# Optimization experiments

Hardware: AMD Instinct MI355X
Metric: run time of the kernel (lower is better)

Reference implementation:

```python
import jax, jax.numpy as jnp
import numpy as np

N_STEPS = 96
BATCH = 16384
N_MAT = 8
N_STRIKES = 8
PERIOD = 12          # N_steps // n_maturities
T_HORIZON = 1.0
RFR = 0.03
S0 = 1.0
LAYER = 128
DT = T_HORIZON / N_STEPS
SQRT_DT = float(np.sqrt(DT))
DF = float(np.exp(-RFR * DT))  # per-step discount factor


def _mlp(Win, bin_, Wh, bh, Wout, bout, x, out_fn):
    # x: [features, batch]; linear layers act on axis 0 (matches torch cat along dim 0)
    h = jax.nn.leaky_relu(Win @ x + bin_[:, None])
    for k in range(Wh.shape[0]):
        h = jax.nn.leaky_relu(Wh[k] @ h + bh[k][:, None])
    return out_fn(Wout @ h + bout[:, None])


def _forward(normals, strikes, lev_Win, lev_bin, lev_Wh, lev_bh, lev_Wout, lev_bout,
             hed_Win, hed_bin, hed_Wh, hed_bh, hed_Wout, hed_bout):
    B = normals.shape[1]
    dt = jnp.float32(DT)
    sqrt_dt = jnp.float32(SQRT_DT)
    r = jnp.float32(RFR)
    df = jnp.float32(DF)
    sg = jax.lax.stop_gradient

    def body(carry, xs):
        S_prev, hedging, prices, variance = carry
        i, nn_i = xs                      # i: int32 step (1..N_STEPS), nn_i: [B] normals
        i_f = i.astype(jnp.float32)
        idx = (i - 1) // PERIOD           # which per-period MLP
        t = ((i_f - 1.0) * dt) * jnp.ones((1, B), jnp.float32)
        X = jnp.concatenate([t, S_prev], axis=0)          # [2, B]
        lev = _mlp(lev_Win[idx], lev_bin[idx], lev_Wh[idx], lev_bh[idx],
                   lev_Wout[idx], lev_bout[idx], X, jax.nn.softplus)  # [1, B]
        drift = S_prev * r / (1.0 + jnp.abs(sg(S_prev) * r) * sqrt_dt)
        diffusion = S_prev * lev / (1.0 + jnp.abs(sg(S_prev * lev)) * sqrt_dt)
        dW = sqrt_dt * nn_i                               # [B]
        S_curr = S_prev + drift * dt + diffusion * dW     # [1, B]
        Xh = jnp.concatenate([t, sg(S_prev)], axis=0)
        hedge = _mlp(hed_Win[idx], hed_bin[idx], hed_Wh[idx], hed_bh[idx],
                     hed_Wout[idx], hed_bout[idx], Xh,
                     lambda y: y).reshape(N_STRIKES, N_MAT, B)
        hedging = hedging + (df ** (i_f - 1.0)) * sg(S_prev * diffusion) * hedge * dW
        # maturity handling (maturities at steps PERIOD, 2*PERIOD, ..., N_STEPS)
        table_idx = jnp.clip(i // PERIOD - 1, 0, N_MAT - 1)
        is_mat = (i % PERIOD == 0).astype(jnp.float32)
        simulated = (df ** i_f) * jnp.maximum(S_curr - strikes[:, None], 0.0) \
                    - hedging[:, table_idx]               # [K, B]
        mean = simulated.mean(axis=1)                     # [K]
        var = jnp.sum((simulated - mean[:, None]) ** 2, axis=1) / (B - 1)  # unbiased, as torch .var()
        prices = prices.at[:, table_idx].add(is_mat * mean)
        variance = variance.at[:, table_idx].add(is_mat * var)
        return (S_curr, hedging, prices, variance), None

    body = jax.checkpoint(body)
    carry0 = (jnp.full((1, B), jnp.float32(S0)),
              jnp.zeros((N_STRIKES, N_MAT, B), jnp.float32),
              jnp.zeros((N_STRIKES, N_MAT), jnp.float32),
              jnp.zeros((N_STRIKES, N_MAT), jnp.float32))
    xs = (jnp.arange(1, N_STEPS + 1, dtype=jnp.int32), normals)
    (_, _, prices, variance), _ = jax.lax.scan(body, carry0, xs)
    return prices, variance


def setup_inputs() -> dict:
    key = jax.random.key(0)
    ks = jax.random.split(key, 16)
    M, L, NH = N_MAT, LAYER, 3  # num_layers=4 -> 3 hidden-to-hidden layers

    def w(k, shape, fan_in):
        return (jax.random.normal(k, shape, jnp.float32) / np.sqrt(fan_in)).astype(jnp.float32)

    inp = {
        "normals": jax.random.normal(ks[0], (N_STEPS, BATCH), jnp.float32),
        "strikes": jnp.linspace(0.8, 1.15, N_STRIKES, dtype=jnp.float32),
        "lev_Win": w(ks[1], (M, L, 2), 2),
        "lev_bin": w(ks[2], (M, L), L),
        "lev_Wh": w(ks[3], (M, NH, L, L), L),
        "lev_bh": w(ks[4], (M, NH, L), L),
        "lev_Wout": w(ks[5], (M, 1, L), L),
        "lev_bout": w(ks[6], (M, 1), L),
        "hed_Win": w(ks[7], (M, L, 2), 2),
        "hed_bin": w(ks[8], (M, L), L),
        "hed_Wh": w(ks[9], (M, NH, L, L), L),
        "hed_bh": w(ks[10], (M, NH, L), L),
        "hed_Wout": w(ks[11], (M, N_STRIKES * N_MAT, L), L),
        "hed_bout": w(ks[12], (M, N_STRIKES * N_MAT), L),
    }
    return inp


def reference(normals, strikes, lev_Win, lev_bin, lev_Wh, lev_bh, lev_Wout, lev_bout,
              hed_Win, hed_bin, hed_Wh, hed_bh, hed_Wout, hed_bout):
    return _forward(normals, strikes, lev_Win, lev_bin, lev_Wh, lev_bh, lev_Wout, lev_bout,
                    hed_Win, hed_bin, hed_Wh, hed_bh, hed_Wout, hed_bout)
```

## Files before the change

kernel.cpp:

```cpp
#include <hip/hip_runtime.h>
#include <math.h>

typedef __attribute__((ext_vector_type(8)))  short  short8;
typedef __attribute__((ext_vector_type(4)))  short  short4v;
typedef __attribute__((ext_vector_type(16))) float  f32x16;
typedef __attribute__((ext_vector_type(4)))  float  f32x4v;

#define DT_F    ((float)(1.0/96.0))
#define SQDT_F  (0.10206207261596575f)
#define DF_F    (0.99968754882437816f)
#define RFR_F   (0.03f)

#define SWZ(c,k) (((c)<<7) + ((k) ^ (((c)&15)<<3)))

static __device__ __forceinline__ short f2bf(float x) {
    return __builtin_bit_cast(short, (__bf16)x);
}
static __device__ __forceinline__ float bf2f(short h) {
    return (float)__builtin_bit_cast(__bf16, h);
}

__device__ __forceinline__ void layer1(const float* __restrict__ Win, const float* __restrict__ bin_,
        float t, const float* __restrict__ sScur, ushort* __restrict__ out, int wvm, int l)
{
    const int g = l >> 4, c15 = l & 15;
    const int r0 = (wvm << 5) + (g << 3);
    float a8[8], w1[8];
#pragma unroll
    for (int jj = 0; jj < 8; ++jj) {
        const int r = r0 + jj;
        a8[jj] = fmaf(Win[2*r], t, bin_[r]);
        w1[jj] = Win[2*r + 1];
    }
#pragma unroll
    for (int cc = 0; cc < 4; ++cc) {
        const int c = c15 + (cc << 4);
        const float S = sScur[c];
        short8 v;
#pragma unroll
        for (int jj = 0; jj < 8; ++jj) {
            float h = fmaf(w1[jj], S, a8[jj]);
            h = fmaxf(h, 0.01f * h);
            v[jj] = f2bf(h);
        }
        *(short8*)&out[SWZ(c, r0)] = v;
    }
}

__device__ __forceinline__ void hidden32(const ushort* __restrict__ WFm, const float* __restrict__ bias,
        const ushort* __restrict__ bin, ushort* __restrict__ bout, int wvm, int l)
{
    const int c0 = l & 31;
    const int l5 = l >> 5;
    const int kr = l5 << 3;
    f32x16 a0e = {0,0,0,0,0,0,0,0,0,0,0,0,0,0,0,0};
    f32x16 a0o = a0e, a1e = a0e, a1o = a0e;
    const short8* fb = (const short8*)(WFm + (wvm << 12));
#pragma unroll
    for (int kc = 0; kc < 8; kc += 2) {
        short8 aE = fb[kc * 64 + l];
        short8 aO = fb[(kc + 1) * 64 + l];
        const int k0e = (kc << 4) + kr;
        const int k0o = k0e + 16;
        short8 b0e = *(const short8*)&bin[SWZ(c0,      k0e)];
        short8 b1e = *(const short8*)&bin[SWZ(c0 + 32, k0e)];
        short8 b0o = *(const short8*)&bin[SWZ(c0,      k0o)];
        short8 b1o = *(const short8*)&bin[SWZ(c0 + 32, k0o)];
        a0e = __builtin_amdgcn_mfma_f32_32x32x16_bf16(aE, b0e, a0e, 0, 0, 0);
        a1e = __builtin_amdgcn_mfma_f32_32x32x16_bf16(aE, b1e, a1e, 0, 0, 0);
        a0o = __builtin_amdgcn_mfma_f32_32x32x16_bf16(aO, b0o, a0o, 0, 0, 0);
        a1o = __builtin_amdgcn_mfma_f32_32x32x16_bf16(aO, b1o, a1o, 0, 0, 0);
    }
    const f32x16 acc0 = a0e + a0o;
    const f32x16 acc1 = a1e + a1o;
#pragma unroll
    for (int q = 0; q < 4; ++q) {
        const int rloc = (q << 3) + (l5 << 2);
        const f32x4v bq = *(const f32x4v*)&bias[(wvm << 5) + rloc];
        short4v o0, o1;
#pragma unroll
        for (int ii = 0; ii < 4; ++ii) {
            float x0 = acc0[(q << 2) + ii] + bq[ii]; o0[ii] = f2bf(fmaxf(x0, 0.01f * x0));
            float x1 = acc1[(q << 2) + ii] + bq[ii]; o1[ii] = f2bf(fmaxf(x1, 0.01f * x1));
        }
        *(short4v*)&bout[SWZ(c0,      (wvm << 5) + rloc)] = o0;
        *(short4v*)&bout[SWZ(c0 + 32, (wvm << 5) + rloc)] = o1;
    }
}

__global__ __launch_bounds__(512, 2)
void sim_kernel(const float* __restrict__ normals, const float* __restrict__ strikes,
                const float* __restrict__ levWin, const float* __restrict__ levbin,
                const float* __restrict__ levbh,  const float* __restrict__ levWout,
                const float* __restrict__ levbout,
                const float* __restrict__ hedWin, const float* __restrict__ hedbin,
                const float* __restrict__ hedbh,  const float* __restrict__ hedbout,
                const ushort* __restrict__ WF, double* __restrict__ accD)
{
    __shared__ ushort bufL[2][64 * 128];
    __shared__ ushort bufH[2][64 * 128];
    __shared__ float  sS[2][64];
    __shared__ float  sHc[64];

    const int tid  = threadIdx.x;
    const int wv   = tid >> 6;
    const int half = wv >> 2;
    const int wvm  = wv & 3;
    const int l    = tid & 63;
    const int g    = l >> 4;
    const int c15  = l & 15;
    const int bp0  = blockIdx.x * 64;

    if (tid < 64) sS[0][tid] = 1.0f;
    float hedg[4][4];
#pragma unroll
    for (int a = 0; a < 4; ++a)
#pragma unroll
        for (int b = 0; b < 4; ++b) hedg[a][b] = 0.f;
    float dfim1 = 1.0f;
    __syncthreads();

    for (int i = 1; i <= 96; ++i) {
        const int idx = (i - 1) / 12;
        const float t = (float)(i - 1) * DT_F;
        const float* sScur = sS[(i - 1) & 1];
        float* sSnxt = sS[i & 1];
        const ushort* WFi = WF + (size_t)idx * 106496;

        ushort* A = half ? bufH[0] : bufL[0];
        ushort* B = half ? bufH[1] : bufL[1];
        const float* Win  = (half ? hedWin : levWin) + idx * 256;
        const float* binp = (half ? hedbin : levbin) + (idx << 7);
        const float* bh   = (half ? hedbh  : levbh)  + idx * 384;
        const ushort* Wm  = WFi + ((half * 3) << 14);

        layer1(Win, binp, t, sScur, A, wvm, l);
        float nrm = 0.f;
        if (half == 0) nrm = normals[(size_t)(i - 1) * 16384 + bp0 + c15 + (wvm << 4)];
        __syncthreads();
        hidden32(Wm,              bh,       A, B, wvm, l);
        __syncthreads();
        hidden32(Wm + 16384,      bh + 128, B, A, wvm, l);
        __syncthreads();
        hidden32(Wm + 32768,      bh + 256, A, B, wvm, l);
        __syncthreads();

        const float dfi = dfim1 * DF_F;
        f32x4v acc0 = {0,0,0,0}, acc1 = acc0, acc2 = acc0, acc3 = acc0;
        if (half == 0) {
            const float* Wo = levWout + (idx << 7);
            float wk[32];
#pragma unroll
            for (int kb = 0; kb < 8; ++kb)
                *(f32x4v*)&wk[4 * kb] = *(const f32x4v*)&Wo[(g << 5) + (kb << 2)];
            const int c = c15 + (wvm << 4);
            float p = 0.f;
#pragma unroll
            for (int kb = 0; kb < 4; ++kb) {
                short8 hv = *(const short8*)&bufL[1][SWZ(c, (g << 5) + (kb << 3))];
#pragma unroll
                for (int j = 0; j < 8; ++j) p = fmaf(bf2f(hv[j]), wk[(kb << 3) + j], p);
            }
            p += __shfl_xor(p, 16);
            p += __shfl_xor(p, 32);
            p += levbout[idx];
            const float lv = (p > 20.f) ? p : __logf(1.f + __expf(p));
            const float S = sScur[c];
            const float drift = S * RFR_F / (1.f + fabsf(S * RFR_F) * SQDT_F);
            const float dif   = S * lv    / (1.f + fabsf(S * lv)   * SQDT_F);
            const float dW = SQDT_F * nrm;
            const float Sn = S + drift * DT_F + dif * dW;
            if (g == 0) { sSnxt[c] = Sn; sHc[c] = dfim1 * (S * dif) * dW; }
        } else {
            const short8* fb = (const short8*)(WFi + 98304 + (wvm << 11));
            __builtin_amdgcn_s_setprio(1);
#pragma unroll
            for (int kcq = 0; kcq < 4; ++kcq) {
                short8 a = fb[kcq * 64 + l];
                const int k0 = (kcq << 5) + (g << 3);
                short8 b0 = *(const short8*)&bufH[1][SWZ(c15,      k0)];
                short8 b1 = *(const short8*)&bufH[1][SWZ(16 + c15, k0)];
                short8 b2 = *(const short8*)&bufH[1][SWZ(32 + c15, k0)];
                short8 b3 = *(const short8*)&bufH[1][SWZ(48 + c15, k0)];
                acc0 = __builtin_amdgcn_mfma_f32_16x16x32_bf16(a, b0, acc0, 0, 0, 0);
                acc1 = __builtin_amdgcn_mfma_f32_16x16x32_bf16(a, b1, acc1, 0, 0, 0);
                acc2 = __builtin_amdgcn_mfma_f32_16x16x32_bf16(a, b2, acc2, 0, 0, 0);
                acc3 = __builtin_amdgcn_mfma_f32_16x16x32_bf16(a, b3, acc3, 0, 0, 0);
            }
            __builtin_amdgcn_s_setprio(0);
        }
        __syncthreads();

        if (half == 1) {
            const f32x4v bo4 = *(const f32x4v*)&hedbout[(idx << 6) + (wvm << 4) + (g << 2)];
            const float hc0 = sHc[c15], hc1 = sHc[16 + c15], hc2 = sHc[32 + c15], hc3 = sHc[48 + c15];
#pragma unroll
            for (int ii = 0; ii < 4; ++ii) {
                hedg[0][ii] = fmaf(hc0, acc0[ii] + bo4[ii], hedg[0][ii]);
                hedg[1][ii] = fmaf(hc1, acc1[ii] + bo4[ii], hedg[1][ii]);
                hedg[2][ii] = fmaf(hc2, acc2[ii] + bo4[ii], hedg[2][ii]);
                hedg[3][ii] = fmaf(hc3, acc3[ii] + bo4[ii], hedg[3][ii]);
            }
            if ((i % 12) == 0) {
                const int m = i / 12 - 1;
                const int isel = m & 3;
                const bool active = ((m >> 2) == (g & 1));
                const int ks = (wvm << 1) + (g >> 1);
                float s_ = 0.f, q_ = 0.f;
                if (active) {
                    const float K = strikes[ks];
#pragma unroll
                    for (int ct = 0; ct < 4; ++ct) {
                        const float* hrow = hedg[ct];
                        const float hv = (isel == 0) ? hrow[0] : (isel == 1) ? hrow[1]
                                        : (isel == 2) ? hrow[2] : hrow[3];
                        const float Sn = sSnxt[(ct << 4) + c15];
                        const float sim = dfi * fmaxf(Sn - K, 0.f) - hv;
                        s_ += sim; q_ += sim * sim;
                    }
                }
#pragma unroll
                for (int off = 1; off < 16; off <<= 1) {
                    s_ += __shfl_xor(s_, off);
                    q_ += __shfl_xor(q_, off);
                }
                if (active && c15 == 0) {
                    const int rep = blockIdx.x & 31;
                    atomicAdd(&accD[rep * 128 + ks * 8 + m], (double)s_);
                    atomicAdd(&accD[rep * 128 + 64 + ks * 8 + m], (double)q_);
                }
            }
        }
        dfim1 = dfi;
    }
}

__global__ void prep_kernel(const float* __restrict__ levWh, const float* __restrict__ hedWh,
                            const float* __restrict__ hedWout,
                            ushort* __restrict__ WF, double* __restrict__ accD)
{
    const long long stride = (long long)gridDim.x * blockDim.x;
    const long long t0 = (long long)blockIdx.x * blockDim.x + threadIdx.x;
    for (long long e = t0; e < 851968LL; e += stride) {
        const int idx = (int)(e / 106496);
        const int rem = (int)(e % 106496);
        float val;
        if (rem < 98304) {
            const int m    = rem >> 14;
            const int r2   = rem & 16383;
            const int slot = r2 >> 9;
            const int rb   = slot >> 3;
            const int kc   = slot & 7;
            const int lane = (r2 >> 3) & 63;
            const int j    = r2 & 7;
            const int r = (rb << 5) + (lane & 31);
            const int k = (kc << 4) + ((lane >> 5) << 3) + j;
            const float* src = (m < 3) ? levWh : hedWh;
            const int mm = (m < 3) ? m : m - 3;
            val = src[(((idx * 3 + mm) << 7) + r) * 128 + k];
        } else {
            const int r3   = rem - 98304;
            const int slot = r3 >> 9;
            const int rb   = slot >> 2;
            const int kcq  = slot & 3;
            const int lane = (r3 >> 3) & 63;
            const int j    = r3 & 7;
            const int r = (rb << 4) + (lane & 15);
            const int k = (kcq << 5) + ((lane >> 4) << 3) + j;
            val = hedWout[(idx << 13) + (r << 7) + k];
        }
        WF[e] = (ushort)f2bf(val);
    }
    for (long long e = t0; e < 4096; e += stride) accD[e] = 0.0;
}

__global__ void finalize_kernel(const double* __restrict__ accD, float* __restrict__ out)
{
    const int t = threadIdx.x;
    if (t < 64) {
        double s = 0.0, q = 0.0;
        for (int rep = 0; rep < 32; ++rep) {
            s += accD[rep * 128 + t];
            q += accD[rep * 128 + 64 + t];
        }
        out[t]      = (float)(s / 16384.0);
        out[64 + t] = (float)((q - s * s / 16384.0) / 16383.0);
    }
}

extern "C" void kernel_launch(void* const* d_in, const int* in_sizes, int n_in,
                              void* d_out, int out_size, void* d_ws, size_t ws_size,
                              hipStream_t stream)
{
    const float* normals = (const float*)d_in[0];
    const float* strikes = (const float*)d_in[1];
    const float* levWin  = (const float*)d_in[2];
    const float* levbin  = (const float*)d_in[3];
    const float* levWh   = (const float*)d_in[4];
    const float* levbh   = (const float*)d_in[5];
    const float* levWout = (const float*)d_in[6];
    const float* levbout = (const float*)d_in[7];
    const float* hedWin  = (const float*)d_in[8];
    const float* hedbin  = (const float*)d_in[9];
    const float* hedWh   = (const float*)d_in[10];
    const float* hedbh   = (const float*)d_in[11];
    const float* hedWout = (const float*)d_in[12];
    const float* hedbout = (const float*)d_in[13];

    ushort* WF   = (ushort*)d_ws;
    double* accD = (double*)((char*)d_ws + 1703936);

    prep_kernel<<<1024, 256, 0, stream>>>(levWh, hedWh, hedWout, WF, accD);
    sim_kernel<<<256, 512, 0, stream>>>(normals, strikes,
                                        levWin, levbin, levbh, levWout, levbout,
                                        hedWin, hedbin, hedbh, hedbout,
                                        WF, accD);
    finalize_kernel<<<1, 64, 0, stream>>>(accD, (float*)d_out);
}
```

Before: 552.2 us.

## Precompute swizzled LDS addresses in a flat buffer and fold bias into MFMA accumulators

Replaces the separate shared arrays and the per-access SWZ macro with one flat byte buffer. Per-lane read and write offsets are precomputed once before the time loop, so each LDS access becomes base plus a compile-time immediate. A new XOR swizzle pattern is meant to avoid bank conflicts for the 32x32 and 16x16 MFMA operand reads. Hidden-layer bias is now loaded as the initial accumulator value instead of being added in the epilogue, which trims per-step address arithmetic and VALU work at the cost of more live registers for the offset arrays.

```diff
diff --git a/kernel.cpp b/kernel.cpp
--- a/kernel.cpp
+++ b/kernel.cpp
@@ -11,7 +11,10 @@
 #define DF_F    (0.99968754882437816f)
 #define RFR_F   (0.03f)
 
-#define SWZ(c,k) (((c)<<7) + ((k) ^ (((c)&15)<<3)))
+#define LDS_L1  32768
+#define LDS_H1  49152
+#define LDS_SS  65536
+#define LDS_HC  66048
 
 static __device__ __forceinline__ short f2bf(float x) {
     return __builtin_bit_cast(short, (__bf16)x);
@@ -19,9 +22,15 @@
 static __device__ __forceinline__ float bf2f(short h) {
     return (float)__builtin_bit_cast(__bf16, h);
 }
+static __device__ __forceinline__ short8 ldsr16(const char* p) {
+    return *(const short8*)__builtin_assume_aligned(p, 16);
+}
+static __device__ __forceinline__ void ldsw8(char* p, short4v v) {
+    *(short4v*)__builtin_assume_aligned(p, 8) = v;
+}
 
 __device__ __forceinline__ void layer1(const float* __restrict__ Win, const float* __restrict__ bin_,
-        float t, const float* __restrict__ sScur, ushort* __restrict__ out, int wvm, int l)
+        float t, const float* __restrict__ sScur, char* __restrict__ lds, int wl1, int wvm, int l)
 {
     const int g = l >> 4, c15 = l & 15;
     const int r0 = (wvm << 5) + (g << 3);
@@ -34,8 +43,7 @@
     }
 #pragma unroll
     for (int cc = 0; cc < 4; ++cc) {
-        const int c = c15 + (cc << 4);
-        const float S = sScur[c];
+        const float S = sScur[c15 + (cc << 4)];
         short8 v;
 #pragma unroll
         for (int jj = 0; jj < 8; ++jj) {
@@ -43,29 +51,37 @@
             h = fmaxf(h, 0.01f * h);
             v[jj] = f2bf(h);
         }
-        *(short8*)&out[SWZ(c, r0)] = v;
-    }
-}
-
-__device__ __forceinline__ void hidden32(const ushort* __restrict__ WFm, const float* __restrict__ bias,
-        const ushort* __restrict__ bin, ushort* __restrict__ bout, int wvm, int l)
-{
-    const int c0 = l & 31;
-    const int l5 = l >> 5;
-    const int kr = l5 << 3;
-    f32x16 a0e = {0,0,0,0,0,0,0,0,0,0,0,0,0,0,0,0};
-    f32x16 a0o = a0e, a1e = a0e, a1o = a0e;
+        *(short8*)__builtin_assume_aligned(lds + wl1 + (cc << 12), 16) = v;
+    }
+}
+
+__device__ __forceinline__ void hidden32(char* __restrict__ lds,
+        const int (&__restrict__ rdk)[8], const int (&__restrict__ wrq)[4],
+        int rdImm, int wrImm,
+        const ushort* __restrict__ WFm, const float* __restrict__ bias,
+        int wvm, int l, int l5)
+{
+    f32x16 a0e, a1e;
+    f32x16 a0o = {0,0,0,0,0,0,0,0,0,0,0,0,0,0,0,0};
+    f32x16 a1o = a0o;
+#pragma unroll
+    for (int q = 0; q < 4; ++q) {
+        const f32x4v bq = *(const f32x4v*)&bias[(wvm << 5) + (q << 3) + (l5 << 2)];
+#pragma unroll
+        for (int ii = 0; ii < 4; ++ii) {
+            a0e[(q << 2) + ii] = bq[ii];
+            a1e[(q << 2) + ii] = bq[ii];
+        }
+    }
     const short8* fb = (const short8*)(WFm + (wvm << 12));
 #pragma unroll
     for (int kc = 0; kc < 8; kc += 2) {
         short8 aE = fb[kc * 64 + l];
         short8 aO = fb[(kc + 1) * 64 + l];
-        const int k0e = (kc << 4) + kr;
-        const int k0o = k0e + 16;
-        short8 b0e = *(const short8*)&bin[SWZ(c0,      k0e)];
-        short8 b1e = *(const short8*)&bin[SWZ(c0 + 32, k0e)];
-        short8 b0o = *(const short8*)&bin[SWZ(c0,      k0o)];
-        short8 b1o = *(const short8*)&bin[SWZ(c0 + 32, k0o)];
+        short8 b0e = ldsr16(lds + rdk[kc]     + rdImm);
+        short8 b1e = ldsr16(lds + rdk[kc]     + rdImm + 8192);
+        short8 b0o = ldsr16(lds + rdk[kc + 1] + rdImm);
+        short8 b1o = ldsr16(lds + rdk[kc + 1] + rdImm + 8192);
         a0e = __builtin_amdgcn_mfma_f32_32x32x16_bf16(aE, b0e, a0e, 0, 0, 0);
         a1e = __builtin_amdgcn_mfma_f32_32x32x16_bf16(aE, b1e, a1e, 0, 0, 0);
         a0o = __builtin_amdgcn_mfma_f32_32x32x16_bf16(aO, b0o, a0o, 0, 0, 0);
@@ -75,16 +91,14 @@
     const f32x16 acc1 = a1e + a1o;
 #pragma unroll
     for (int q = 0; q < 4; ++q) {
-        const int rloc = (q << 3) + (l5 << 2);
-        const f32x4v bq = *(const f32x4v*)&bias[(wvm << 5) + rloc];
         short4v o0, o1;
 #pragma unroll
         for (int ii = 0; ii < 4; ++ii) {
-            float x0 = acc0[(q << 2) + ii] + bq[ii]; o0[ii] = f2bf(fmaxf(x0, 0.01f * x0));
-            float x1 = acc1[(q << 2) + ii] + bq[ii]; o1[ii] = f2bf(fmaxf(x1, 0.01f * x1));
-        }
-        *(short4v*)&bout[SWZ(c0,      (wvm << 5) + rloc)] = o0;
-        *(short4v*)&bout[SWZ(c0 + 32, (wvm << 5) + rloc)] = o1;
+            float x0 = acc0[(q << 2) + ii]; o0[ii] = f2bf(fmaxf(x0, 0.01f * x0));
+            float x1 = acc1[(q << 2) + ii]; o1[ii] = f2bf(fmaxf(x1, 0.01f * x1));
+        }
+        ldsw8(lds + wrq[q] + wrImm,        o0);
+        ldsw8(lds + wrq[q] + wrImm + 8192, o1);
     }
 }
 
@@ -97,10 +111,9 @@
                 const float* __restrict__ hedbh,  const float* __restrict__ hedbout,
                 const ushort* __restrict__ WF, double* __restrict__ accD)
 {
-    __shared__ ushort bufL[2][64 * 128];
-    __shared__ ushort bufH[2][64 * 128];
-    __shared__ float  sS[2][64];
-    __shared__ float  sHc[64];
+    __shared__ char lds[66560];
+    float* sSb = (float*)(lds + LDS_SS);
+    float* sHc = (float*)(lds + LDS_HC);
 
     const int tid  = threadIdx.x;
     const int wv   = tid >> 6;
@@ -109,9 +122,37 @@
     const int l    = tid & 63;
     const int g    = l >> 4;
     const int c15  = l & 15;
+    const int c0   = l & 31;
+    const int l5   = l >> 5;
     const int bp0  = blockIdx.x * 64;
 
-    if (tid < 64) sS[0][tid] = 1.0f;
+    const int chainoff = half << 14;
+    const int rbase = chainoff + (c0 << 8) + ((l5 ^ (c0 & 1)) << 4);
+    const int pxor  = ((c0 >> 1) & 7) << 5;
+    int rdk[8];
+#pragma unroll
+    for (int kc = 0; kc < 8; ++kc) rdk[kc] = rbase + ((kc << 5) ^ pxor);
+    int wrq[4];
+#pragma unroll
+    for (int q = 0; q < 4; ++q)
+        wrq[q] = chainoff + (c0 << 8) + (l5 << 3)
+               + ((q ^ (c0 & 3)) << 4) + ((wvm ^ ((c0 >> 2) & 3)) << 6);
+    const int wl1 = chainoff + (c15 << 8) + ((g ^ (c15 & 3)) << 4)
+                  + ((wvm ^ ((c15 >> 2) & 3)) << 6);
+    int rout[4];
+    if (half == 0) {
+        const int cl = c15 + (wvm << 4);
+        const int ob = LDS_L1 + (cl << 8) + ((g ^ ((cl >> 2) & 3)) << 6);
+#pragma unroll
+        for (int kb = 0; kb < 4; ++kb) rout[kb] = ob + ((kb ^ (cl & 3)) << 4);
+    } else {
+        const int ob = LDS_H1 + (c15 << 8) + (((l >> 4) ^ (c15 & 3)) << 4);
+        const int px2 = ((c15 >> 2) & 3) << 6;
+#pragma unroll
+        for (int kcq = 0; kcq < 4; ++kcq) rout[kcq] = ob + ((kcq << 6) ^ px2);
+    }
+
+    if (tid < 64) sSb[tid] = 1.0f;
     float hedg[4][4];
 #pragma unroll
     for (int a = 0; a < 4; ++a)
@@ -123,26 +164,24 @@
     for (int i = 1; i <= 96; ++i) {
         const int idx = (i - 1) / 12;
         const float t = (float)(i - 1) * DT_F;
-        const float* sScur = sS[(i - 1) & 1];
-        float* sSnxt = sS[i & 1];
+        const float* sScur = sSb + (((i - 1) & 1) << 6);
+        float* sSnxt = sSb + ((i & 1) << 6);
         const ushort* WFi = WF + (size_t)idx * 106496;
 
-        ushort* A = half ? bufH[0] : bufL[0];
-        ushort* B = half ? bufH[1] : bufL[1];
         const float* Win  = (half ? hedWin : levWin) + idx * 256;
         const float* binp = (half ? hedbin : levbin) + (idx << 7);
         const float* bh   = (half ? hedbh  : levbh)  + idx * 384;
         const ushort* Wm  = WFi + ((half * 3) << 14);
 
-        layer1(Win, binp, t, sScur, A, wvm, l);
+        layer1(Win, binp, t, sScur, lds, wl1, wvm, l);
         float nrm = 0.f;
         if (half == 0) nrm = normals[(size_t)(i - 1) * 16384 + bp0 + c15 + (wvm << 4)];
         __syncthreads();
-        hidden32(Wm,              bh,       A, B, wvm, l);
-        __syncthreads();
-        hidden32(Wm + 16384,      bh + 128, B, A, wvm, l);
-        __syncthreads();
-        hidden32(Wm + 32768,      bh + 256, A, B, wvm, l);
+        hidden32(lds, rdk, wrq, 0,     32768, Wm,         bh,       wvm, l, l5);
+        __syncthreads();
+        hidden32(lds, rdk, wrq, 32768, 0,     Wm + 16384, bh + 128, wvm, l, l5);
+        __syncthreads();
+        hidden32(lds, rdk, wrq, 0,     32768, Wm + 32768, bh + 256, wvm, l, l5);
         __syncthreads();
 
         const float dfi = dfim1 * DF_F;
@@ -157,7 +196,7 @@
             float p = 0.f;
 #pragma unroll
             for (int kb = 0; kb < 4; ++kb) {
-                short8 hv = *(const short8*)&bufL[1][SWZ(c, (g << 5) + (kb << 3))];
+                short8 hv = ldsr16(lds + rout[kb]);
 #pragma unroll
                 for (int j = 0; j < 8; ++j) p = fmaf(bf2f(hv[j]), wk[(kb << 3) + j], p);
             }
@@ -177,11 +216,10 @@
 #pragma unroll
             for (int kcq = 0; kcq < 4; ++kcq) {
                 short8 a = fb[kcq * 64 + l];
-                const int k0 = (kcq << 5) + (g << 3);
-                short8 b0 = *(const short8*)&bufH[1][SWZ(c15,      k0)];
-                short8 b1 = *(const short8*)&bufH[1][SWZ(16 + c15, k0)];
-                short8 b2 = *(const short8*)&bufH[1][SWZ(32 + c15, k0)];
-                short8 b3 = *(const short8*)&bufH[1][SWZ(48 + c15, k0)];
+                short8 b0 = ldsr16(lds + rout[kcq]);
+                short8 b1 = ldsr16(lds + rout[kcq] + 4096);
+                short8 b2 = ldsr16(lds + rout[kcq] + 8192);
+                short8 b3 = ldsr16(lds + rout[kcq] + 12288);
                 acc0 = __builtin_amdgcn_mfma_f32_16x16x32_bf16(a, b0, acc0, 0, 0, 0);
                 acc1 = __builtin_amdgcn_mfma_f32_16x16x32_bf16(a, b1, acc1, 0, 0, 0);
                 acc2 = __builtin_amdgcn_mfma_f32_16x16x32_bf16(a, b2, acc2, 0, 0, 0);
```

New measurement: 564.9 us. +2.3%, slower.
